# Kernel tuning notes

Measured on AMD Instinct MI355X. Metric: run time of the kernel, lower is better.

Reference implementation:

```python
import jax, jax.numpy as jnp
import numpy as np

EMB_DIM = 1024
HEAD = 16
HEAD_DIM = EMB_DIM // HEAD


def setup_inputs() -> dict:
    key = jax.random.key(0)
    ks = jax.random.split(key, 6)
    s = 1.0 / np.sqrt(EMB_DIM)
    return {
        "z": jax.random.normal(ks[0], (4, 2048, EMB_DIM), dtype=jnp.float32),
        "w_q": jax.random.normal(ks[1], (EMB_DIM, EMB_DIM), dtype=jnp.float32) * s,
        "w_k": jax.random.normal(ks[2], (EMB_DIM, EMB_DIM), dtype=jnp.float32) * s,
        "w_v": jax.random.normal(ks[3], (EMB_DIM, EMB_DIM), dtype=jnp.float32) * s,
        "w_o": jax.random.normal(ks[4], (EMB_DIM, EMB_DIM), dtype=jnp.float32) * s,
        "b_o": jax.random.normal(ks[5], (EMB_DIM,), dtype=jnp.float32) * 0.01,
    }


def reference(z, w_q, w_k, w_v, w_o, b_o):
    B, N, D = z.shape
    # QKV projections (nn.Linear: x @ W.T; here weights stored as (D_in, D_out))
    q = (z @ w_q).reshape(B, N, HEAD, HEAD_DIM).transpose(0, 2, 1, 3)  # bhnd
    k = (z @ w_k).reshape(B, N, HEAD, HEAD_DIM).transpose(0, 2, 1, 3)
    v = (z @ w_v).reshape(B, N, HEAD, HEAD_DIM).transpose(0, 2, 1, 3)
    scale = 1.0 / np.sqrt(HEAD_DIM).astype(np.float32)
    dots = jnp.einsum("bhnd,bhmd->bhnm", q, k) * scale
    attn = jax.nn.softmax(dots, axis=-1)
    out = jnp.einsum("bhnm,bhmd->bhnd", attn, v)
    out = out.transpose(0, 2, 1, 3).reshape(B, N, D)
    return out @ w_o + b_o
```

## Files before the change

kernel.cpp:

```cpp
#include <hip/hip_runtime.h>
#include <hip/hip_bf16.h>
#include <stdint.h>

typedef unsigned short u16;
typedef __attribute__((ext_vector_type(8))) short bf16x8;
typedef __attribute__((ext_vector_type(4))) float f32x4;

static __device__ inline u16 f2bf(float f) {
  union { float f; uint32_t u; } v; v.f = f;
  uint32_t u = v.u;
  u += 0x7fffu + ((u >> 16) & 1);
  return (u16)(u >> 16);
}

static __device__ inline uint32_t pack_bf16(float lo, float hi) {
  union { float f; uint32_t u; } a, b;
  a.f = lo; b.f = hi;
  uint32_t ua = a.u + 0x8000u;
  uint32_t ub = b.u + 0x8000u;
  return __builtin_amdgcn_perm(ub, ua, 0x07060302u);
}

__global__ __launch_bounds__(256) void cast_bf16_kernel(const float* __restrict__ src,
                                                        u16* __restrict__ dst, int n4) {
  int i = blockIdx.x * 256 + threadIdx.x;
  if (i < n4) {
    float4 v = reinterpret_cast<const float4*>(src)[i];
    uint2 o;
    o.x = (uint32_t)f2bf(v.x) | ((uint32_t)f2bf(v.y) << 16);
    o.y = (uint32_t)f2bf(v.z) | ((uint32_t)f2bf(v.w) << 16);
    reinterpret_cast<uint2*>(dst)[i] = o;
  }
}

__global__ __launch_bounds__(256) void wtrans_kernel(const float* __restrict__ wq,
                                                     const float* __restrict__ wk,
                                                     const float* __restrict__ wv,
                                                     const float* __restrict__ wo,
                                                     u16* __restrict__ bqkv,
                                                     u16* __restrict__ wot) {
  int z = blockIdx.z;
  const float* src = (z == 0) ? wq : (z == 1) ? wk : (z == 2) ? wv : wo;
  u16* dst = (z < 3) ? (bqkv + (size_t)z * 1024 * 1024) : wot;
  __shared__ float tile[32][33];
  int c0 = blockIdx.x * 32, r0 = blockIdx.y * 32;
  int tx = threadIdx.x, ty = threadIdx.y;
#pragma unroll
  for (int i = 0; i < 32; i += 8)
    tile[ty + i][tx] = src[(size_t)(r0 + ty + i) * 1024 + c0 + tx];
  __syncthreads();
#pragma unroll
  for (int i = 0; i < 32; i += 8)
    dst[(size_t)(c0 + ty + i) * 1024 + r0 + tx] = f2bf(tile[tx][ty + i]);
}

__global__ __launch_bounds__(256) void vtrans_kernel(const u16* __restrict__ V,
                                                     u16* __restrict__ Vt) {
  int bh = blockIdx.y;
  int k0 = blockIdx.x * 64;
  __shared__ __align__(16) u16 tile[64][72];
  int tid = threadIdx.x;
  int row = tid >> 3, c8 = (tid & 7) * 8;
  const u16* src = V + ((size_t)bh * 2048 + k0) * 64;
  *reinterpret_cast<uint4*>(&tile[row][c8]) =
      *reinterpret_cast<const uint4*>(src + row * 64 + c8);
  *reinterpret_cast<uint4*>(&tile[row + 32][c8]) =
      *reinterpret_cast<const uint4*>(src + (row + 32) * 64 + c8);
  __syncthreads();
  u16* dst = Vt + (size_t)bh * 64 * 2048 + k0;
#pragma unroll
  for (int half = 0; half < 64; half += 32) {
    int dim = row + half;
    union { u16 s[8]; uint4 v; } tmp;
#pragma unroll
    for (int i = 0; i < 8; i++) tmp.s[i] = tile[c8 + i][dim];
    *reinterpret_cast<uint4*>(dst + (size_t)dim * 2048 + c8) = tmp.v;
  }
}

template <int MODE>
__global__ __launch_bounds__(256) void gemm_bt_kernel(
    const u16* __restrict__ A, const u16* __restrict__ Bt,
    u16* __restrict__ outQ, u16* __restrict__ outK, u16* __restrict__ outV,
    float* __restrict__ outC, const float* __restrict__ bias) {
  const int Kd = 1024;
  const int n0 = blockIdx.x * 128;
  const int m0 = blockIdx.y * 128;
  __shared__ __align__(16) u16 Asm[128 * 40];
  __shared__ __align__(16) u16 Bsm[128 * 40];
  const int tid = threadIdx.x;
  const int wave = tid >> 6, lane = tid & 63;
  const int quad = lane >> 4, l15 = lane & 15;
  const int wm = (wave >> 1) * 64, wn = (wave & 1) * 64;
  const int srow = tid >> 2, spart = tid & 3;

  f32x4 acc[4][4] = {};

  for (int k0 = 0; k0 < Kd; k0 += 32) {
    __syncthreads();
    uint4 a0 = *reinterpret_cast<const uint4*>(A + (size_t)(m0 + srow) * Kd + k0 + spart * 8);
    uint4 a1 = *reinterpret_cast<const uint4*>(A + (size_t)(m0 + srow + 64) * Kd + k0 + spart * 8);
    uint4 b0 = *reinterpret_cast<const uint4*>(Bt + (size_t)(n0 + srow) * Kd + k0 + spart * 8);
    uint4 b1 = *reinterpret_cast<const uint4*>(Bt + (size_t)(n0 + srow + 64) * Kd + k0 + spart * 8);
    *reinterpret_cast<uint4*>(Asm + srow * 40 + spart * 8) = a0;
    *reinterpret_cast<uint4*>(Asm + (srow + 64) * 40 + spart * 8) = a1;
    *reinterpret_cast<uint4*>(Bsm + srow * 40 + spart * 8) = b0;
    *reinterpret_cast<uint4*>(Bsm + (srow + 64) * 40 + spart * 8) = b1;
    __syncthreads();
    bf16x8 af[4], bf[4];
#pragma unroll
    for (int i = 0; i < 4; i++)
      af[i] = *reinterpret_cast<const bf16x8*>(Asm + (wm + i * 16 + l15) * 40 + quad * 8);
#pragma unroll
    for (int i = 0; i < 4; i++)
      bf[i] = *reinterpret_cast<const bf16x8*>(Bsm + (wn + i * 16 + l15) * 40 + quad * 8);
#pragma unroll
    for (int mi = 0; mi < 4; mi++)
#pragma unroll
      for (int ni = 0; ni < 4; ni++)
        acc[mi][ni] = __builtin_amdgcn_mfma_f32_16x16x32_bf16(af[mi], bf[ni], acc[mi][ni], 0, 0, 0);
  }

  if (MODE == 0) {
#pragma unroll
    for (int mi = 0; mi < 4; mi++)
#pragma unroll
      for (int ni = 0; ni < 4; ni++) {
        int n = n0 + wn + ni * 16 + l15;
        int which = n >> 10;
        int hn = n & 1023;
        int h = hn >> 6, dim = hn & 63;
        u16* dst = (which == 0) ? outQ : (which == 1) ? outK : outV;
        float qscale = (which == 0) ? 0.125f : 1.0f;
#pragma unroll
        for (int r = 0; r < 4; r++) {
          int m = m0 + wm + mi * 16 + quad * 4 + r;
          int b = m >> 11, tok = m & 2047;
          dst[(((size_t)(b * 16 + h)) * 2048 + tok) * 64 + dim] = f2bf(acc[mi][ni][r] * qscale);
        }
      }
  } else {
#pragma unroll
    for (int mi = 0; mi < 4; mi++)
#pragma unroll
      for (int ni = 0; ni < 4; ni++) {
        int n = n0 + wn + ni * 16 + l15;
        float bv = bias[n];
#pragma unroll
        for (int r = 0; r < 4; r++) {
          int m = m0 + wm + mi * 16 + quad * 4 + r;
          outC[(size_t)m * 1024 + n] = acc[mi][ni][r] + bv;
        }
      }
  }
}

__global__ __launch_bounds__(256) void attn_kernel(const u16* __restrict__ Q,
                                                   const u16* __restrict__ K,
                                                   const u16* __restrict__ Vt,
                                                   u16* __restrict__ Oout) {
  const int bh = blockIdx.y;
  const int q0 = blockIdx.x * 64;
  const int tid = threadIdx.x;
  const int wave = tid >> 6, lane = tid & 63;
  const int quad = lane >> 4, l15 = lane & 15;

  __shared__ __align__(16) u16 Qs[64 * 72];
  __shared__ __align__(16) u16 Ks[64 * 72];
  __shared__ __align__(16) u16 Vs[64 * 72];
  __shared__ __align__(16) u16 Ps[4][16 * 72];

  const u16* Qg = Q + ((size_t)bh * 2048 + q0) * 64;
  const u16* Kg = K + (size_t)bh * 2048 * 64;
  const u16* Vg = Vt + (size_t)bh * 64 * 2048;

  for (int c = tid; c < 512; c += 256) {
    int row = c >> 3, col = (c & 7) * 8;
    *reinterpret_cast<uint4*>(&Qs[row * 72 + col]) =
        *reinterpret_cast<const uint4*>(Qg + row * 64 + col);
  }
  __syncthreads();
  bf16x8 qf0, qf1;
  {
    const int qrow = wave * 16 + l15;
    qf0 = *reinterpret_cast<const bf16x8*>(&Qs[qrow * 72 + quad * 8]);
    qf1 = *reinterpret_cast<const bf16x8*>(&Qs[qrow * 72 + 32 + quad * 8]);
  }

  float lsum = 0.f;
  f32x4 oacc[4] = {};
  u16* Pw = &Ps[wave][0];

  for (int kt = 0; kt < 2048; kt += 64) {
    __syncthreads();
    for (int c = tid; c < 512; c += 256) {
      int row = c >> 3, col = (c & 7) * 8;
      *reinterpret_cast<uint4*>(&Ks[row * 72 + col]) =
          *reinterpret_cast<const uint4*>(Kg + (size_t)(kt + row) * 64 + col);
      *reinterpret_cast<uint4*>(&Vs[row * 72 + col]) =
          *reinterpret_cast<const uint4*>(Vg + (size_t)row * 2048 + kt + col);
    }
    __syncthreads();

#pragma unroll
    for (int f = 0; f < 4; f++) {
      bf16x8 kf0 = *reinterpret_cast<const bf16x8*>(&Ks[(f * 16 + l15) * 72 + quad * 8]);
      bf16x8 kf1 = *reinterpret_cast<const bf16x8*>(&Ks[(f * 16 + l15) * 72 + 32 + quad * 8]);
      f32x4 t = {};
      t = __builtin_amdgcn_mfma_f32_16x16x32_bf16(kf0, qf0, t, 0, 0, 0);
      t = __builtin_amdgcn_mfma_f32_16x16x32_bf16(kf1, qf1, t, 0, 0, 0);
      float p0 = __expf(fminf(t[0], 30.f));
      float p1 = __expf(fminf(t[1], 30.f));
      float p2 = __expf(fminf(t[2], 30.f));
      float p3 = __expf(fminf(t[3], 30.f));
      lsum += (p0 + p1) + (p2 + p3);
      uint2 pk;
      pk.x = pack_bf16(p0, p1);
      pk.y = pack_bf16(p2, p3);
      *reinterpret_cast<uint2*>(&Pw[l15 * 72 + f * 16 + quad * 4]) = pk;
    }

    bf16x8 pf0 = *reinterpret_cast<const bf16x8*>(&Pw[l15 * 72 + quad * 8]);
    bf16x8 pf1 = *reinterpret_cast<const bf16x8*>(&Pw[l15 * 72 + 32 + quad * 8]);
#pragma unroll
    for (int f = 0; f < 4; f++) {
      bf16x8 vf0 = *reinterpret_cast<const bf16x8*>(&Vs[(f * 16 + l15) * 72 + quad * 8]);
      bf16x8 vf1 = *reinterpret_cast<const bf16x8*>(&Vs[(f * 16 + l15) * 72 + 32 + quad * 8]);
      oacc[f] = __builtin_amdgcn_mfma_f32_16x16x32_bf16(pf0, vf0, oacc[f], 0, 0, 0);
      oacc[f] = __builtin_amdgcn_mfma_f32_16x16x32_bf16(pf1, vf1, oacc[f], 0, 0, 0);
    }
  }

  lsum += __shfl_xor(lsum, 16, 64);
  lsum += __shfl_xor(lsum, 32, 64);
  float inv[4];
#pragma unroll
  for (int r = 0; r < 4; r++)
    inv[r] = 1.0f / __shfl(lsum, quad * 4 + r, 64);

  const int b = bh >> 4, h = bh & 15;
  u16* dst = Oout + (size_t)b * 2048 * 1024 + (size_t)h * 64;
#pragma unroll
  for (int f = 0; f < 4; f++)
#pragma unroll
    for (int r = 0; r < 4; r++) {
      int q = q0 + wave * 16 + quad * 4 + r;
      dst[(size_t)q * 1024 + f * 16 + l15] = f2bf(oacc[f][r] * inv[r]);
    }
}

extern "C" void kernel_launch(void* const* d_in, const int* in_sizes, int n_in,
                              void* d_out, int out_size, void* d_ws, size_t ws_size,
                              hipStream_t stream) {
  (void)in_sizes; (void)n_in; (void)out_size; (void)ws_size;
  const float* z  = (const float*)d_in[0];
  const float* wq = (const float*)d_in[1];
  const float* wk = (const float*)d_in[2];
  const float* wv = (const float*)d_in[3];
  const float* wo = (const float*)d_in[4];
  const float* bo = (const float*)d_in[5];
  float* out = (float*)d_out;

  char* ws = (char*)d_ws;
  u16* zb   = (u16*)(ws);
  u16* bqkv = (u16*)(ws + (16ull << 20));
  u16* wot  = (u16*)(ws + (22ull << 20));
  u16* Qb   = (u16*)(ws + (24ull << 20));
  u16* Kb   = (u16*)(ws + (40ull << 20));
  u16* Vb   = (u16*)(ws + (56ull << 20));
  u16* Vtb  = (u16*)(ws + (72ull << 20));
  u16* Ob   = zb;

  cast_bf16_kernel<<<8192, 256, 0, stream>>>(z, zb, 2097152);
  wtrans_kernel<<<dim3(32, 32, 4), dim3(32, 8), 0, stream>>>(wq, wk, wv, wo, bqkv, wot);
  gemm_bt_kernel<0><<<dim3(24, 64), 256, 0, stream>>>(zb, bqkv, Qb, Kb, Vb, nullptr, nullptr);
  vtrans_kernel<<<dim3(32, 64), 256, 0, stream>>>(Vb, Vtb);
  attn_kernel<<<dim3(32, 64), 256, 0, stream>>>(Qb, Kb, Vtb, Ob);
  gemm_bt_kernel<1><<<dim3(8, 64), 256, 0, stream>>>(Ob, wot, nullptr, nullptr, nullptr, out, bo);
}
```

Measured before the change: 342.5 us.

## Write V transposed from QKV GEMM and retile attention to 32x32 MFMA

The QKV projection epilogue now writes V directly in transposed layout, which removes the separate V transpose kernel and its extra memory round trip. The attention kernel is restructured to handle 128 queries per block using 32x32x16 MFMA instructions. It reuses the Q shared buffer for the P tile, folds log2(e) into the Q scale so it can use exp2f, and drops the clamp. This aims to raise MFMA efficiency and K/V reuse per block, at the cost of more registers and the loss of overflow protection on the exponent.

New measurement: 334.2 us. -2.4%, faster.

```diff
diff --git a/kernel.cpp b/kernel.cpp
--- a/kernel.cpp
+++ b/kernel.cpp
@@ -5,6 +5,7 @@
 typedef unsigned short u16;
 typedef __attribute__((ext_vector_type(8))) short bf16x8;
 typedef __attribute__((ext_vector_type(4))) float f32x4;
+typedef __attribute__((ext_vector_type(16))) float f32x16;
 
 static __device__ inline u16 f2bf(float f) {
   union { float f; uint32_t u; } v; v.f = f;
@@ -54,34 +55,10 @@
     dst[(size_t)(c0 + ty + i) * 1024 + r0 + tx] = f2bf(tile[tx][ty + i]);
 }
 
-__global__ __launch_bounds__(256) void vtrans_kernel(const u16* __restrict__ V,
-                                                     u16* __restrict__ Vt) {
-  int bh = blockIdx.y;
-  int k0 = blockIdx.x * 64;
-  __shared__ __align__(16) u16 tile[64][72];
-  int tid = threadIdx.x;
-  int row = tid >> 3, c8 = (tid & 7) * 8;
-  const u16* src = V + ((size_t)bh * 2048 + k0) * 64;
-  *reinterpret_cast<uint4*>(&tile[row][c8]) =
-      *reinterpret_cast<const uint4*>(src + row * 64 + c8);
-  *reinterpret_cast<uint4*>(&tile[row + 32][c8]) =
-      *reinterpret_cast<const uint4*>(src + (row + 32) * 64 + c8);
-  __syncthreads();
-  u16* dst = Vt + (size_t)bh * 64 * 2048 + k0;
-#pragma unroll
-  for (int half = 0; half < 64; half += 32) {
-    int dim = row + half;
-    union { u16 s[8]; uint4 v; } tmp;
-#pragma unroll
-    for (int i = 0; i < 8; i++) tmp.s[i] = tile[c8 + i][dim];
-    *reinterpret_cast<uint4*>(dst + (size_t)dim * 2048 + c8) = tmp.v;
-  }
-}
-
 template <int MODE>
 __global__ __launch_bounds__(256) void gemm_bt_kernel(
     const u16* __restrict__ A, const u16* __restrict__ Bt,
-    u16* __restrict__ outQ, u16* __restrict__ outK, u16* __restrict__ outV,
+    u16* __restrict__ outQ, u16* __restrict__ outK, u16* __restrict__ outVt,
     float* __restrict__ outC, const float* __restrict__ bias) {
   const int Kd = 1024;
   const int n0 = blockIdx.x * 128;
@@ -122,21 +99,30 @@
   }
 
   if (MODE == 0) {
+    const int which = (n0 + wn) >> 10;
 #pragma unroll
     for (int mi = 0; mi < 4; mi++)
 #pragma unroll
       for (int ni = 0; ni < 4; ni++) {
         int n = n0 + wn + ni * 16 + l15;
-        int which = n >> 10;
         int hn = n & 1023;
         int h = hn >> 6, dim = hn & 63;
-        u16* dst = (which == 0) ? outQ : (which == 1) ? outK : outV;
-        float qscale = (which == 0) ? 0.125f : 1.0f;
-#pragma unroll
-        for (int r = 0; r < 4; r++) {
-          int m = m0 + wm + mi * 16 + quad * 4 + r;
+        if (which == 2) {
+          int m = m0 + wm + mi * 16 + quad * 4;
           int b = m >> 11, tok = m & 2047;
-          dst[(((size_t)(b * 16 + h)) * 2048 + tok) * 64 + dim] = f2bf(acc[mi][ni][r] * qscale);
+          uint2 pk;
+          pk.x = pack_bf16(acc[mi][ni][0], acc[mi][ni][1]);
+          pk.y = pack_bf16(acc[mi][ni][2], acc[mi][ni][3]);
+          *reinterpret_cast<uint2*>(outVt + ((size_t)(b * 16 + h) * 64 + dim) * 2048 + tok) = pk;
+        } else {
+          u16* dst = (which == 0) ? outQ : outK;
+          float qscale = (which == 0) ? 0.1803368801111204f : 1.0f;
+#pragma unroll
+          for (int r = 0; r < 4; r++) {
+            int m = m0 + wm + mi * 16 + quad * 4 + r;
+            int b = m >> 11, tok = m & 2047;
+            dst[(((size_t)(b * 16 + h)) * 2048 + tok) * 64 + dim] = f2bf(acc[mi][ni][r] * qscale);
+          }
         }
       }
   } else {
@@ -155,45 +141,46 @@
   }
 }
 
-__global__ __launch_bounds__(256) void attn_kernel(const u16* __restrict__ Q,
-                                                   const u16* __restrict__ K,
-                                                   const u16* __restrict__ Vt,
-                                                   u16* __restrict__ Oout) {
+__global__ __launch_bounds__(256, 4) void attn_kernel(const u16* __restrict__ Q,
+                                                      const u16* __restrict__ K,
+                                                      const u16* __restrict__ Vt,
+                                                      u16* __restrict__ Oout) {
   const int bh = blockIdx.y;
-  const int q0 = blockIdx.x * 64;
+  const int q0 = blockIdx.x * 128;
   const int tid = threadIdx.x;
   const int wave = tid >> 6, lane = tid & 63;
-  const int quad = lane >> 4, l15 = lane & 15;
-
-  __shared__ __align__(16) u16 Qs[64 * 72];
+  const int l31 = lane & 31, h = lane >> 5;
+
+  __shared__ __align__(16) u16 QPs[128 * 72];
   __shared__ __align__(16) u16 Ks[64 * 72];
   __shared__ __align__(16) u16 Vs[64 * 72];
-  __shared__ __align__(16) u16 Ps[4][16 * 72];
 
   const u16* Qg = Q + ((size_t)bh * 2048 + q0) * 64;
   const u16* Kg = K + (size_t)bh * 2048 * 64;
   const u16* Vg = Vt + (size_t)bh * 64 * 2048;
 
-  for (int c = tid; c < 512; c += 256) {
+#pragma unroll
+  for (int k = 0; k < 4; k++) {
+    int c = tid + k * 256;
     int row = c >> 3, col = (c & 7) * 8;
-    *reinterpret_cast<uint4*>(&Qs[row * 72 + col]) =
+    *reinterpret_cast<uint4*>(&QPs[row * 72 + col]) =
         *reinterpret_cast<const uint4*>(Qg + row * 64 + col);
   }
   __syncthreads();
-  bf16x8 qf0, qf1;
-  {
-    const int qrow = wave * 16 + l15;
-    qf0 = *reinterpret_cast<const bf16x8*>(&Qs[qrow * 72 + quad * 8]);
-    qf1 = *reinterpret_cast<const bf16x8*>(&Qs[qrow * 72 + 32 + quad * 8]);
-  }
-
+  bf16x8 qf[4];
+#pragma unroll
+  for (int dc = 0; dc < 4; dc++)
+    qf[dc] = *reinterpret_cast<const bf16x8*>(&QPs[(wave * 32 + l31) * 72 + dc * 16 + h * 8]);
+
+  u16* Pw = &QPs[wave * 32 * 72];
   float lsum = 0.f;
-  f32x4 oacc[4] = {};
-  u16* Pw = &Ps[wave][0];
+  f32x16 oacc[2] = {};
 
   for (int kt = 0; kt < 2048; kt += 64) {
     __syncthreads();
-    for (int c = tid; c < 512; c += 256) {
+#pragma unroll
+    for (int k = 0; k < 2; k++) {
+      int c = tid + k * 256;
       int row = c >> 3, col = (c & 7) * 8;
       *reinterpret_cast<uint4*>(&Ks[row * 72 + col]) =
           *reinterpret_cast<const uint4*>(Kg + (size_t)(kt + row) * 64 + col);
@@ -203,49 +190,58 @@
     __syncthreads();
 
 #pragma unroll
-    for (int f = 0; f < 4; f++) {
-      bf16x8 kf0 = *reinterpret_cast<const bf16x8*>(&Ks[(f * 16 + l15) * 72 + quad * 8]);
-      bf16x8 kf1 = *reinterpret_cast<const bf16x8*>(&Ks[(f * 16 + l15) * 72 + 32 + quad * 8]);
-      f32x4 t = {};
-      t = __builtin_amdgcn_mfma_f32_16x16x32_bf16(kf0, qf0, t, 0, 0, 0);
-      t = __builtin_amdgcn_mfma_f32_16x16x32_bf16(kf1, qf1, t, 0, 0, 0);
-      float p0 = __expf(fminf(t[0], 30.f));
-      float p1 = __expf(fminf(t[1], 30.f));
-      float p2 = __expf(fminf(t[2], 30.f));
-      float p3 = __expf(fminf(t[3], 30.f));
-      lsum += (p0 + p1) + (p2 + p3);
-      uint2 pk;
-      pk.x = pack_bf16(p0, p1);
-      pk.y = pack_bf16(p2, p3);
-      *reinterpret_cast<uint2*>(&Pw[l15 * 72 + f * 16 + quad * 4]) = pk;
-    }
-
-    bf16x8 pf0 = *reinterpret_cast<const bf16x8*>(&Pw[l15 * 72 + quad * 8]);
-    bf16x8 pf1 = *reinterpret_cast<const bf16x8*>(&Pw[l15 * 72 + 32 + quad * 8]);
-#pragma unroll
-    for (int f = 0; f < 4; f++) {
-      bf16x8 vf0 = *reinterpret_cast<const bf16x8*>(&Vs[(f * 16 + l15) * 72 + quad * 8]);
-      bf16x8 vf1 = *reinterpret_cast<const bf16x8*>(&Vs[(f * 16 + l15) * 72 + 32 + quad * 8]);
-      oacc[f] = __builtin_amdgcn_mfma_f32_16x16x32_bf16(pf0, vf0, oacc[f], 0, 0, 0);
-      oacc[f] = __builtin_amdgcn_mfma_f32_16x16x32_bf16(pf1, vf1, oacc[f], 0, 0, 0);
-    }
-  }
-
-  lsum += __shfl_xor(lsum, 16, 64);
+    for (int kb = 0; kb < 2; kb++) {
+      f32x16 s = {};
+#pragma unroll
+      for (int dc = 0; dc < 4; dc++) {
+        bf16x8 kf = *reinterpret_cast<const bf16x8*>(&Ks[(kb * 32 + l31) * 72 + dc * 16 + h * 8]);
+        s = __builtin_amdgcn_mfma_f32_32x32x16_bf16(kf, qf[dc], s, 0, 0, 0);
+      }
+      float p[16];
+#pragma unroll
+      for (int i = 0; i < 16; i++) p[i] = exp2f(s[i]);
+#pragma unroll
+      for (int i = 0; i < 16; i++) lsum += p[i];
+#pragma unroll
+      for (int rg = 0; rg < 4; rg++) {
+        uint2 pk;
+        pk.x = pack_bf16(p[rg * 4 + 0], p[rg * 4 + 1]);
+        pk.y = pack_bf16(p[rg * 4 + 2], p[rg * 4 + 3]);
+        *reinterpret_cast<uint2*>(&Pw[l31 * 72 + kb * 32 + rg * 8 + h * 4]) = pk;
+      }
+    }
+
+    bf16x8 pf[4];
+#pragma unroll
+    for (int kc = 0; kc < 4; kc++)
+      pf[kc] = *reinterpret_cast<const bf16x8*>(&Pw[l31 * 72 + kc * 16 + h * 8]);
+#pragma unroll
+    for (int dt = 0; dt < 2; dt++) {
+#pragma unroll
+      for (int kc = 0; kc < 4; kc++) {
+        bf16x8 vf = *reinterpret_cast<const bf16x8*>(&Vs[(dt * 32 + l31) * 72 + kc * 16 + h * 8]);
+        oacc[dt] = __builtin_amdgcn_mfma_f32_32x32x16_bf16(pf[kc], vf, oacc[dt], 0, 0, 0);
+      }
+    }
+  }
+
   lsum += __shfl_xor(lsum, 32, 64);
-  float inv[4];
-#pragma unroll
-  for (int r = 0; r < 4; r++)
-    inv[r] = 1.0f / __shfl(lsum, quad * 4 + r, 64);
-
-  const int b = bh >> 4, h = bh & 15;
-  u16* dst = Oout + (size_t)b * 2048 * 1024 + (size_t)h * 64;
-#pragma unroll
-  for (int f = 0; f < 4; f++)
-#pragma unroll
-    for (int r = 0; r < 4; r++) {
-      int q = q0 + wave * 16 + quad * 4 + r;
-      dst[(size_t)q * 1024 + f * 16 + l15] = f2bf(oacc[f][r] * inv[r]);
+  float inv[16];
+#pragma unroll
+  for (int reg = 0; reg < 16; reg++) {
+    int qq = (reg & 3) + 8 * (reg >> 2) + 4 * h;
+    int lv = __builtin_amdgcn_ds_bpermute(qq << 2, __float_as_int(lsum));
+    inv[reg] = __builtin_amdgcn_rcpf(__int_as_float(lv));
+  }
+
+  const int b = bh >> 4, hd = bh & 15;
+  u16* dst = Oout + (size_t)b * 2048 * 1024 + (size_t)hd * 64;
+#pragma unroll
+  for (int dt = 0; dt < 2; dt++)
+#pragma unroll
+    for (int reg = 0; reg < 16; reg++) {
+      int qq = q0 + wave * 32 + (reg & 3) + 8 * (reg >> 2) + 4 * h;
+      dst[(size_t)qq * 1024 + dt * 32 + l31] = f2bf(oacc[dt][reg] * inv[reg]);
     }
 }
 
@@ -267,14 +263,12 @@
   u16* wot  = (u16*)(ws + (22ull << 20));
   u16* Qb   = (u16*)(ws + (24ull << 20));
   u16* Kb   = (u16*)(ws + (40ull << 20));
-  u16* Vb   = (u16*)(ws + (56ull << 20));
-  u16* Vtb  = (u16*)(ws + (72ull << 20));
+  u16* Vtb  = (u16*)(ws + (56ull << 20));
   u16* Ob   = zb;
 
   cast_bf16_kernel<<<8192, 256, 0, stream>>>(z, zb, 2097152);
   wtrans_kernel<<<dim3(32, 32, 4), dim3(32, 8), 0, stream>>>(wq, wk, wv, wo, bqkv, wot);
-  gemm_bt_kernel<0><<<dim3(24, 64), 256, 0, stream>>>(zb, bqkv, Qb, Kb, Vb, nullptr, nullptr);
-  vtrans_kernel<<<dim3(32, 64), 256, 0, stream>>>(Vb, Vtb);
-  attn_kernel<<<dim3(32, 64), 256, 0, stream>>>(Qb, Kb, Vtb, Ob);
+  gemm_bt_kernel<0><<<dim3(24, 64), 256, 0, stream>>>(zb, bqkv, Qb, Kb, Vtb, nullptr, nullptr);
+  attn_kernel<<<dim3(16, 64), 256, 0, stream>>>(Qb, Kb, Vtb, Ob);
   gemm_bt_kernel<1><<<dim3(8, 64), 256, 0, stream>>>(Ob, wot, nullptr, nullptr, nullptr, out, bo);
 }
```
